# Optimization experiments

Measured on AMD Instinct MI355X. Metric: run time of the kernel, lower is better.

The kernel has to match this reference:

```python
import jax, jax.numpy as jnp
import numpy as np

S, N, C, E, L = 4, 50000, 256, 800000, 3
EPS = 1e-5  # nn.LayerNorm default eps


def setup_inputs() -> dict:
    key = jax.random.key(0)
    ks = jax.random.split(key, 10)
    sc = 1.0 / np.sqrt(C)
    x = jax.random.normal(ks[0], (S, N, C), jnp.float32)
    edge_index = jax.random.randint(ks[1], (S, 2, E), 0, N, dtype=jnp.int32)
    edge_weight = jax.random.uniform(ks[2], (S, E), jnp.float32)
    W_gcn = jax.random.uniform(ks[3], (L, C, C), jnp.float32, -sc, sc)
    b_gcn = jnp.zeros((L, C), jnp.float32)
    ln_scale = jnp.ones((L, C), jnp.float32)
    ln_bias = jnp.zeros((L, C), jnp.float32)
    w_ih = jax.random.uniform(ks[4], (3 * C, C), jnp.float32, -sc, sc)
    w_hh = jax.random.uniform(ks[5], (3 * C, C), jnp.float32, -sc, sc)
    b_ih = jax.random.uniform(ks[6], (3 * C,), jnp.float32, -sc, sc)
    b_hh = jax.random.uniform(ks[7], (3 * C,), jnp.float32, -sc, sc)
    return dict(x=x, edge_index=edge_index, edge_weight=edge_weight,
                W_gcn=W_gcn, b_gcn=b_gcn, ln_scale=ln_scale, ln_bias=ln_bias,
                w_ih=w_ih, w_hh=w_hh, b_ih=b_ih, b_hh=b_hh)


def _gcn_conv(h, row, col, ew, W, b):
    """PyG GCNConv: out = D^{-1/2} (A + I) D^{-1/2} (h W) + b, edge weights ew."""
    h = h @ W  # [N, C]
    loop = jnp.arange(N, dtype=row.dtype)
    row = jnp.concatenate([row, loop])
    col = jnp.concatenate([col, loop])
    ew = jnp.concatenate([ew, jnp.ones((N,), ew.dtype)])
    deg = jax.ops.segment_sum(ew, col, num_segments=N)  # in-degree at targets
    dinv = jnp.where(deg > 0, jax.lax.rsqrt(jnp.maximum(deg, EPS * 0 + 1e-12)), 0.0)
    norm = dinv[row] * ew * dinv[col]  # [E+N]
    msg = h[row] * norm[:, None]       # gather from sources
    return jax.ops.segment_sum(msg, col, num_segments=N) + b


def _layernorm(h, scale, bias):
    mu = jnp.mean(h, axis=-1, keepdims=True)
    var = jnp.mean(jnp.square(h - mu), axis=-1, keepdims=True)
    return (h - mu) * jax.lax.rsqrt(var + EPS) * scale + bias


def _snapshot(x, ei, ew, W_gcn, b_gcn, ln_scale, ln_bias):
    h = x
    row, col = ei[0], ei[1]
    for l in range(L):
        h = _gcn_conv(h, row, col, ew, W_gcn[l], b_gcn[l])
        h = _layernorm(h, ln_scale[l], ln_bias[l])
        h = jax.nn.relu(h)  # dropout is identity in eval mode
    return h


def _gru_last(seq, w_ih, w_hh, b_ih, b_hh):
    """seq: [S, N, C] -> final hidden [N, C] (torch single-layer GRU)."""
    def step(h, x_t):
        gi = x_t @ w_ih.T + b_ih
        gh = h @ w_hh.T + b_hh
        i_r, i_z, i_n = jnp.split(gi, 3, axis=-1)
        h_r, h_z, h_n = jnp.split(gh, 3, axis=-1)
        r = jax.nn.sigmoid(i_r + h_r)
        z = jax.nn.sigmoid(i_z + h_z)
        n = jnp.tanh(i_n + r * h_n)
        return (1.0 - z) * n + z * h, None
    h0 = jnp.zeros(seq.shape[1:], seq.dtype)
    h_last, _ = jax.lax.scan(step, h0, seq)
    return h_last


def reference(x, edge_index, edge_weight, W_gcn, b_gcn, ln_scale, ln_bias,
              w_ih, w_hh, b_ih, b_hh):
    feats = jax.vmap(lambda xs, eis, ews: _snapshot(xs, eis, ews, W_gcn, b_gcn, ln_scale, ln_bias))(
        x, edge_index, edge_weight)  # [S, N, C]
    return _gru_last(feats, w_ih, w_hh, b_ih, b_hh)  # [N, C]
```

## Files before the change

### kernel.cpp

```cpp
#include <hip/hip_runtime.h>
#include <cmath>

#define S_ 4
#define N_ 50000
#define C_ 256
#define E_ 800000
#define L_ 3
#define EPS_ 1e-5f
#define CAP_ 64

typedef __attribute__((ext_vector_type(8))) short bf16x8;
typedef __attribute__((ext_vector_type(4))) float f32x4;

__device__ __forceinline__ float bf2f(unsigned short s) {
  return __uint_as_float(((unsigned)s) << 16);
}
__device__ __forceinline__ unsigned short f2bf(float f) {
  unsigned u = __float_as_uint(f);
  return (unsigned short)((u + 0x7fffu + ((u >> 16) & 1u)) >> 16);
}

__device__ __forceinline__ void gload_lds16(const void* g, void* l) {
  __builtin_amdgcn_global_load_lds(
      (const __attribute__((address_space(1))) unsigned int*)g,
      (__attribute__((address_space(3))) unsigned int*)l, 16, 0, 0);
}

__device__ __forceinline__ void swz_block(int id, int nbx, int nby, int& bmi, int& bni) {
  const int NB8 = nby * 8;
  int fullb = (nbx >> 3) * NB8;
  if (id < fullb) {
    int g = id / NB8, pp = id - g * NB8;
    bmi = g * 8 + (pp & 7);
    bni = pp >> 3;
  } else {
    int rem = nbx & 7;
    int idp = id - fullb;
    bmi = (nbx & ~7) + idp % rem;
    bni = idp / rem;
  }
}

template<bool AF32>
__global__ __launch_bounds__(256) void gemm_bf16_kernel(
    const unsigned short* __restrict__ A, const float* __restrict__ Af,
    const unsigned short* __restrict__ Bt,
    unsigned short* __restrict__ Cout, int M, int Nn, int K, int nby)
{
  __shared__ alignas(16) unsigned short As[2][128 * 32];
  __shared__ alignas(16) unsigned short Bs[2][128 * 32];
  const int tid = threadIdx.x;
  const int lane = tid & 63;
  const int wid = tid >> 6;
  const int wr = wid >> 1, wc = wid & 1;
  int bmi, bni;
  swz_block(blockIdx.x, gridDim.x / nby, nby, bmi, bni);
  const int bm = bmi * 128, bn = bni * 128;
  const int l15 = lane & 15, l4 = lane >> 4;

  f32x4 acc[4][4] = {};

  int offA[4], offB[4];
  #pragma unroll
  for (int mi = 0; mi < 4; ++mi) {
    int ra = wr * 64 + mi * 16 + l15;
    offA[mi] = ra * 32 + ((l4 ^ ((ra >> 1) & 3)) << 3);
    int rb = wc * 64 + mi * 16 + l15;
    offB[mi] = rb * 32 + ((l4 ^ ((rb >> 1) & 3)) << 3);
  }
  const int rs = tid >> 2;
  const int gs = tid & 3;

  float4 fa[2][2];

  auto loadA_f32 = [&](int k0) {
    #pragma unroll
    for (int t2 = 0; t2 < 2; ++t2) {
      int r = rs + t2 * 64;
      int q = gs ^ ((r >> 1) & 3);
      int arow = bm + r; if (arow >= M) arow = M - 1;
      const float* srcp = &Af[(size_t)arow * K + k0 + q * 8];
      fa[t2][0] = *(const float4*)srcp;
      fa[t2][1] = *(const float4*)(srcp + 4);
    }
  };
  auto writeA_f32 = [&](int buf) {
    #pragma unroll
    for (int t2 = 0; t2 < 2; ++t2) {
      int slot = t2 * 256 + tid;
      union { unsigned short us[8]; bf16x8 v; } u;
      const float* f = (const float*)&fa[t2][0];
      #pragma unroll
      for (int j = 0; j < 8; ++j) u.us[j] = f2bf(f[j]);
      *(bf16x8*)&As[buf][slot * 8] = u.v;
    }
  };
  auto stageA_bf = [&](int buf, int k0) {
    #pragma unroll
    for (int t2 = 0; t2 < 2; ++t2) {
      int r = rs + t2 * 64;
      int q = gs ^ ((r >> 1) & 3);
      int arow = bm + r; if (arow >= M) arow = M - 1;
      gload_lds16(&A[(size_t)arow * K + k0 + q * 8], &As[buf][(t2 * 256 + tid) * 8]);
    }
  };
  auto stageB = [&](int buf, int k0) {
    #pragma unroll
    for (int t2 = 0; t2 < 2; ++t2) {
      int r = rs + t2 * 64;
      int q = gs ^ ((r >> 1) & 3);
      gload_lds16(&Bt[(size_t)(bn + r) * K + k0 + q * 8], &Bs[buf][(t2 * 256 + tid) * 8]);
    }
  };

  const int nt = K >> 5;
  if constexpr (AF32) {
    loadA_f32(0);
    stageB(0, 0);
    writeA_f32(0);
  } else {
    stageA_bf(0, 0);
    stageB(0, 0);
  }
  asm volatile("s_waitcnt vmcnt(0)" ::: "memory");
  __syncthreads();

  int cur = 0;
  for (int t = 0; t < nt; ++t) {
    if (t + 1 < nt) {
      if constexpr (AF32) {
        loadA_f32((t + 1) * 32);
        stageB(cur ^ 1, (t + 1) * 32);
      } else {
        stageA_bf(cur ^ 1, (t + 1) * 32);
        stageB(cur ^ 1, (t + 1) * 32);
      }
    }

    bf16x8 af[4], bfr[4];
    #pragma unroll
    for (int mi = 0; mi < 4; ++mi) af[mi] = *(const bf16x8*)&As[cur][offA[mi]];
    #pragma unroll
    for (int ni = 0; ni < 4; ++ni) bfr[ni] = *(const bf16x8*)&Bs[cur][offB[ni]];
    #pragma unroll
    for (int mi = 0; mi < 4; ++mi)
      #pragma unroll
      for (int ni = 0; ni < 4; ++ni)
        acc[mi][ni] = __builtin_amdgcn_mfma_f32_16x16x32_bf16(
            bfr[ni], af[mi], acc[mi][ni], 0, 0, 0);

    if constexpr (AF32) {
      if (t + 1 < nt) writeA_f32(cur ^ 1);
    }
    asm volatile("s_waitcnt vmcnt(0)" ::: "memory");
    __syncthreads();
    cur ^= 1;
  }

  #pragma unroll
  for (int mi = 0; mi < 4; ++mi) {
    int row = bm + wr * 64 + mi * 16 + l15;
    if (row < M) {
      #pragma unroll
      for (int ni = 0; ni < 4; ++ni) {
        int colb = bn + wc * 64 + ni * 16 + l4 * 4;
        ushort4 o;
        o.x = f2bf(acc[mi][ni][0]);
        o.y = f2bf(acc[mi][ni][1]);
        o.z = f2bf(acc[mi][ni][2]);
        o.w = f2bf(acc[mi][ni][3]);
        *(ushort4*)&Cout[(size_t)row * Nn + colb] = o;
      }
    }
  }
}

__global__ __launch_bounds__(256) void gru_fused_kernel(
    const unsigned short* __restrict__ feat,
    const unsigned short* __restrict__ hq_in,
    const unsigned short* __restrict__ Wp_ih,
    const unsigned short* __restrict__ Wp_hh,
    const float* __restrict__ b_ih, const float* __restrict__ b_hh,
    unsigned short* __restrict__ hq_out, float* __restrict__ hout,
    int first, int M)
{
  __shared__ alignas(16) unsigned short As[2][128 * 32];
  __shared__ alignas(16) unsigned short Bs[2][96 * 32];
  const int tid = threadIdx.x;
  const int lane = tid & 63;
  const int wv = tid >> 6;
  const int l15 = lane & 15, l4 = lane >> 4;

  int bmi, bni;
  swz_block(blockIdx.x, gridDim.x / 8, 8, bmi, bni);
  const int bm = bmi * 128;
  const int c0 = bni * 32;
  const int brow0 = bni * 96;

  f32x4 acc_i[2][6] = {};
  f32x4 acc_h[2][6] = {};

  int offA[2], offB[6];
  #pragma unroll
  for (int mi = 0; mi < 2; ++mi) {
    int ra = wv * 32 + mi * 16 + l15;
    offA[mi] = ra * 32 + ((l4 ^ ((ra >> 1) & 3)) << 3);
  }
  #pragma unroll
  for (int ni = 0; ni < 6; ++ni) {
    int rb = ni * 16 + l15;
    offB[ni] = rb * 32 + ((l4 ^ ((rb >> 1) & 3)) << 3);
  }

  const int nt = first ? 8 : 16;

  auto stage = [&](int buf, int t) {
    int k0 = (t & 7) * 32;
    const unsigned short* Ap = (t < 8) ? feat : hq_in;
    const unsigned short* Bp = (t < 8) ? Wp_ih : Wp_hh;
    #pragma unroll
    for (int t2 = 0; t2 < 2; ++t2) {
      int slot = t2 * 256 + tid;
      int r = slot >> 2;
      int q = (slot & 3) ^ ((r >> 1) & 3);
      int arow = bm + r; if (arow >= M) arow = M - 1;
      gload_lds16(&Ap[(size_t)arow * 256 + k0 + q * 8], &As[buf][slot * 8]);
    }
    {
      int slot = tid;
      int r = slot >> 2;
      int q = (slot & 3) ^ ((r >> 1) & 3);
      gload_lds16(&Bp[(size_t)(brow0 + r) * 256 + k0 + q * 8], &Bs[buf][slot * 8]);
    }
    if (tid < 128) {
      int slot = 256 + tid;
      int r = slot >> 2;
      int q = (slot & 3) ^ ((r >> 1) & 3);
      gload_lds16(&Bp[(size_t)(brow0 + r) * 256 + k0 + q * 8], &Bs[buf][slot * 8]);
    }
  };

  stage(0, 0);
  asm volatile("s_waitcnt vmcnt(0)" ::: "memory");
  __syncthreads();

  int cur = 0;
  for (int t = 0; t < nt; ++t) {
    if (t + 1 < nt) stage(cur ^ 1, t + 1);

    bf16x8 af[2], bfr[6];
    #pragma unroll
    for (int mi = 0; mi < 2; ++mi) af[mi] = *(const bf16x8*)&As[cur][offA[mi]];
    #pragma unroll
    for (int ni = 0; ni < 6; ++ni) bfr[ni] = *(const bf16x8*)&Bs[cur][offB[ni]];
    if (t < 8) {
      #pragma unroll
      for (int mi = 0; mi < 2; ++mi)
        #pragma unroll
        for (int ni = 0; ni < 6; ++ni)
          acc_i[mi][ni] = __builtin_amdgcn_mfma_f32_16x16x32_bf16(
              bfr[ni], af[mi], acc_i[mi][ni], 0, 0, 0);
    } else {
      #pragma unroll
      for (int mi = 0; mi < 2; ++mi)
        #pragma unroll
        for (int ni = 0; ni < 6; ++ni)
          acc_h[mi][ni] = __builtin_amdgcn_mfma_f32_16x16x32_bf16(
              bfr[ni], af[mi], acc_h[mi][ni], 0, 0, 0);
    }

    asm volatile("s_waitcnt vmcnt(0)" ::: "memory");
    __syncthreads();
    cur ^= 1;
  }

  #pragma unroll
  for (int mi = 0; mi < 2; ++mi) {
    int row = bm + wv * 32 + mi * 16 + l15;
    if (row < M) {
      #pragma unroll
      for (int cni = 0; cni < 2; ++cni) {
        int dc = cni * 16 + l4 * 4;
        int c = c0 + dc;
        float4 bir = *(const float4*)&b_ih[c];
        float4 biz = *(const float4*)&b_ih[256 + c];
        float4 bin = *(const float4*)&b_ih[512 + c];
        float4 bhr = *(const float4*)&b_hh[c];
        float4 bhz = *(const float4*)&b_hh[256 + c];
        float4 bhn = *(const float4*)&b_hh[512 + c];
        float hpv[4] = {0.f, 0.f, 0.f, 0.f};
        if (!first) {
          ushort4 hp = *(const ushort4*)&hq_in[(size_t)row * 256 + c];
          hpv[0] = bf2f(hp.x); hpv[1] = bf2f(hp.y);
          hpv[2] = bf2f(hp.z); hpv[3] = bf2f(hp.w);
        }
        const float* pbir = (const float*)&bir; const float* pbiz = (const float*)&biz;
        const float* pbin = (const float*)&bin; const float* pbhr = (const float*)&bhr;
        const float* pbhz = (const float*)&bhz; const float* pbhn = (const float*)&bhn;
        float hv[4];
        #pragma unroll
        for (int rr = 0; rr < 4; ++rr) {
          float gir = acc_i[mi][0 + cni][rr] + pbir[rr];
          float giz = acc_i[mi][2 + cni][rr] + pbiz[rr];
          float gin = acc_i[mi][4 + cni][rr] + pbin[rr];
          float ghr = (first ? 0.f : acc_h[mi][0 + cni][rr]) + pbhr[rr];
          float ghz = (first ? 0.f : acc_h[mi][2 + cni][rr]) + pbhz[rr];
          float ghn = (first ? 0.f : acc_h[mi][4 + cni][rr]) + pbhn[rr];
          float rg = 1.f / (1.f + expf(-(gir + ghr)));
          float zg = 1.f / (1.f + expf(-(giz + ghz)));
          float ng = tanhf(gin + rg * ghn);
          hv[rr] = (1.f - zg) * ng + zg * hpv[rr];
        }
        if (hq_out) {
          ushort4 o;
          o.x = f2bf(hv[0]); o.y = f2bf(hv[1]); o.z = f2bf(hv[2]); o.w = f2bf(hv[3]);
          *(ushort4*)&hq_out[(size_t)row * 256 + c] = o;
        }
        if (hout) {
          float4 o = make_float4(hv[0], hv[1], hv[2], hv[3]);
          *(float4*)&hout[(size_t)row * 256 + c] = o;
        }
      }
    }
  }
}

__global__ void prep_weights_kernel(const float* __restrict__ W_gcn,
                                    const float* __restrict__ w_ih,
                                    const float* __restrict__ w_hh,
                                    unsigned short* __restrict__ wt_gcn,
                                    unsigned short* __restrict__ wp_ih,
                                    unsigned short* __restrict__ wp_hh) {
  int i = blockIdx.x * blockDim.x + threadIdx.x;
  const int LCC = L_ * C_ * C_, WSZ = 768 * C_;
  if (i < LCC) {
    int l = i / (C_ * C_);
    int rem = i - l * C_ * C_;
    int nn = rem >> 8, k = rem & 255;
    wt_gcn[i] = f2bf(W_gcn[l * C_ * C_ + k * C_ + nn]);
  } else if (i < LCC + 2 * WSZ) {
    int j = i - LCC;
    int which = j / WSZ;
    int d = j - which * WSZ;
    int jrow = d >> 8, k = d & 255;
    int chunk = jrow / 96, jj = jrow - chunk * 96;
    int g = jj >> 5, dc = jj & 31;
    int srow = g * 256 + chunk * 32 + dc;
    float v = which ? w_hh[srow * 256 + k] : w_ih[srow * 256 + k];
    (which ? wp_hh : wp_ih)[d] = f2bf(v);
  }
}

__global__ void scatter_fill_kernel(const int* __restrict__ edge_idx,
                                    const float* __restrict__ edge_w,
                                    unsigned long long* __restrict__ recs,
                                    int* __restrict__ cnt_g) {
  int e = blockIdx.x * blockDim.x + threadIdx.x;
  if (e < S_ * E_) {
    int s = e / E_;
    int ee = e - s * E_;
    int r = edge_idx[(size_t)s * 2 * E_ + ee];
    int c = edge_idx[(size_t)s * 2 * E_ + E_ + ee];
    float w = edge_w[(size_t)s * E_ + ee];
    int ng = s * N_ + c;
    int pos = atomicAdd(&cnt_g[ng], 1);
    if (pos < CAP_) {
      recs[((size_t)ng << 6) + pos] =
          ((unsigned long long)__float_as_uint(w) << 32) | (unsigned int)r;
    }
  }
}

__global__ __launch_bounds__(256) void deg_dinv_kernel(
    const unsigned long long* __restrict__ recs, const int* __restrict__ cnt_g,
    float* __restrict__ dinv_g) {
  const int lane = threadIdx.x & 63, wv = threadIdx.x >> 6;
  const int ng = blockIdx.x * 4 + wv;
  int cnt = min(cnt_g[ng], CAP_);
  float w = 0.f;
  if (lane < cnt)
    w = __uint_as_float((unsigned int)(recs[((size_t)ng << 6) + lane] >> 32));
  #pragma unroll
  for (int off = 32; off > 0; off >>= 1) w += __shfl_xor(w, off);
  if (lane == 0) dinv_g[ng] = rsqrtf(w + 1.0f);
}

__global__ void normify_kernel(const unsigned long long* __restrict__ recs,
                               const int* __restrict__ cnt_g,
                               const float* __restrict__ dinv_g,
                               unsigned int* __restrict__ src_norm) {
  int idx = blockIdx.x * blockDim.x + threadIdx.x;
  if (idx < S_ * N_ * CAP_) {
    int ng = idx >> 6, slot = idx & 63;
    int cnt = min(cnt_g[ng], CAP_);
    if (slot < cnt) {
      unsigned long long rec = recs[idx];
      int src = (int)(unsigned int)rec & 0xFFFF;
      float w = __uint_as_float((unsigned int)(rec >> 32));
      int s = ng / N_;
      float nrm = dinv_g[s * N_ + src] * w * dinv_g[ng];
      src_norm[idx] = (unsigned int)src | ((unsigned int)f2bf(nrm) << 16);
    }
  }
}

__global__ __launch_bounds__(256) void spmm_ln_relu_kernel(
    const unsigned short* __restrict__ hW_all, const int* __restrict__ cnt_g,
    const unsigned int* __restrict__ src_norm, const float* __restrict__ dinv_g,
    const float* __restrict__ bgcn, const float* __restrict__ lnsc,
    const float* __restrict__ lnbi, unsigned short* __restrict__ out)
{
  const int tid = threadIdx.x;
  const int lane = tid & 63, wv = tid >> 6;
  const int n_g = blockIdx.x * 4 + wv;
  const int s = n_g / N_;
  const int n = n_g - s * N_;
  const int c4 = lane << 2;
  const unsigned short* hW = hW_all + ((size_t)s * N_ << 8);

  const int cnt = min(cnt_g[n_g], CAP_);
  unsigned int rec = (lane < cnt) ? src_norm[((size_t)n_g << 6) + lane] : 0u;

  float a0, a1, a2, a3;
  {
    float dv = dinv_g[n_g];
    float w = dv * dv;
    ushort4 u = *(const ushort4*)&hW[((size_t)n << 8) + c4];
    a0 = w * bf2f(u.x); a1 = w * bf2f(u.y); a2 = w * bf2f(u.z); a3 = w * bf2f(u.w);
  }
  int j = 0;
  for (; j + 3 < cnt; j += 4) {
    unsigned int r0 = __shfl((int)rec, j + 0);
    unsigned int r1 = __shfl((int)rec, j + 1);
    unsigned int r2 = __shfl((int)rec, j + 2);
    unsigned int r3 = __shfl((int)rec, j + 3);
    ushort4 u0 = *(const ushort4*)&hW[((size_t)(r0 & 0xFFFFu) << 8) + c4];
    ushort4 u1 = *(const ushort4*)&hW[((size_t)(r1 & 0xFFFFu) << 8) + c4];
    ushort4 u2 = *(const ushort4*)&hW[((size_t)(r2 & 0xFFFFu) << 8) + c4];
    ushort4 u3 = *(const ushort4*)&hW[((size_t)(r3 & 0xFFFFu) << 8) + c4];
    float n0 = bf2f((unsigned short)(r0 >> 16));
    float n1 = bf2f((unsigned short)(r1 >> 16));
    float n2 = bf2f((unsigned short)(r2 >> 16));
    float n3 = bf2f((unsigned short)(r3 >> 16));
    a0 = fmaf(n0, bf2f(u0.x), a0); a1 = fmaf(n0, bf2f(u0.y), a1);
    a2 = fmaf(n0, bf2f(u0.z), a2); a3 = fmaf(n0, bf2f(u0.w), a3);
    a0 = fmaf(n1, bf2f(u1.x), a0); a1 = fmaf(n1, bf2f(u1.y), a1);
    a2 = fmaf(n1, bf2f(u1.z), a2); a3 = fmaf(n1, bf2f(u1.w), a3);
    a0 = fmaf(n2, bf2f(u2.x), a0); a1 = fmaf(n2, bf2f(u2.y), a1);
    a2 = fmaf(n2, bf2f(u2.z), a2); a3 = fmaf(n2, bf2f(u2.w), a3);
    a0 = fmaf(n3, bf2f(u3.x), a0); a1 = fmaf(n3, bf2f(u3.y), a1);
    a2 = fmaf(n3, bf2f(u3.z), a2); a3 = fmaf(n3, bf2f(u3.w), a3);
  }
  for (; j < cnt; ++j) {
    unsigned int r0 = __shfl((int)rec, j);
    ushort4 u0 = *(const ushort4*)&hW[((size_t)(r0 & 0xFFFFu) << 8) + c4];
    float n0 = bf2f((unsigned short)(r0 >> 16));
    a0 = fmaf(n0, bf2f(u0.x), a0); a1 = fmaf(n0, bf2f(u0.y), a1);
    a2 = fmaf(n0, bf2f(u0.z), a2); a3 = fmaf(n0, bf2f(u0.w), a3);
  }

  float4 bg = *(const float4*)&bgcn[c4];
  float v0 = a0 + bg.x, v1 = a1 + bg.y, v2 = a2 + bg.z, v3 = a3 + bg.w;
  float s1 = (v0 + v1) + (v2 + v3);
  float s2 = (v0 * v0 + v1 * v1) + (v2 * v2 + v3 * v3);
  #pragma unroll
  for (int off = 32; off > 0; off >>= 1) {
    s1 += __shfl_xor(s1, off);
    s2 += __shfl_xor(s2, off);
  }
  float mu = s1 * (1.0f / C_);
  float var = s2 * (1.0f / C_) - mu * mu;
  float inv = rsqrtf(var + EPS_);
  float4 sc = *(const float4*)&lnsc[c4];
  float4 bi = *(const float4*)&lnbi[c4];
  ushort4 o;
  o.x = f2bf(fmaxf((v0 - mu) * inv * sc.x + bi.x, 0.f));
  o.y = f2bf(fmaxf((v1 - mu) * inv * sc.y + bi.y, 0.f));
  o.z = f2bf(fmaxf((v2 - mu) * inv * sc.z + bi.z, 0.f));
  o.w = f2bf(fmaxf((v3 - mu) * inv * sc.w + bi.w, 0.f));
  *(ushort4*)&out[((size_t)n_g << 8) + c4] = o;
}

extern "C" void kernel_launch(void* const* d_in, const int* in_sizes, int n_in,
                              void* d_out, int out_size, void* d_ws, size_t ws_size,
                              hipStream_t stream) {
  const float* x        = (const float*)d_in[0];
  const int*   edge_idx = (const int*)d_in[1];
  const float* edge_w   = (const float*)d_in[2];
  const float* W_gcn    = (const float*)d_in[3];
  const float* b_gcn    = (const float*)d_in[4];
  const float* ln_scale = (const float*)d_in[5];
  const float* ln_bias  = (const float*)d_in[6];
  const float* w_ih     = (const float*)d_in[7];
  const float* w_hh     = (const float*)d_in[8];
  const float* b_ih     = (const float*)d_in[9];
  const float* b_hh     = (const float*)d_in[10];
  float* h_out = (float*)d_out;

  char* p = (char*)d_ws;
  auto carve = [&](size_t bytes) -> void* {
    void* r = (void*)p;
    p += (bytes + 255) & ~(size_t)255;
    return r;
  };
  unsigned long long* recs = (unsigned long long*)carve((size_t)S_ * N_ * CAP_ * 8);
  unsigned int* src_norm = (unsigned int*)carve((size_t)S_ * N_ * CAP_ * 4);
  int*   cnt_g       = (int*)carve((size_t)S_ * N_ * 4);
  float* dinv_g      = (float*)carve((size_t)S_ * N_ * 4);
  unsigned short* wt_gcn = (unsigned short*)carve((size_t)L_ * C_ * C_ * 2);
  unsigned short* wp_ih  = (unsigned short*)carve((size_t)768 * C_ * 2);
  unsigned short* wp_hh  = (unsigned short*)carve((size_t)768 * C_ * 2);
  unsigned short* hW_all = (unsigned short*)carve((size_t)S_ * N_ * C_ * 2);
  unsigned short* fA_all = (unsigned short*)carve((size_t)S_ * N_ * C_ * 2);
  unsigned short* fB_all = (unsigned short*)carve((size_t)S_ * N_ * C_ * 2);
  unsigned short* hq0    = (unsigned short*)carve((size_t)N_ * C_ * 2);
  unsigned short* hq1    = (unsigned short*)carve((size_t)N_ * C_ * 2);

  const int TB = 256;

  hipMemsetAsync(cnt_g, 0, (size_t)S_ * N_ * 4, stream);

  const int PREP_N = L_ * C_ * C_ + 2 * 768 * C_;
  prep_weights_kernel<<<(PREP_N + TB - 1) / TB, TB, 0, stream>>>(
      W_gcn, w_ih, w_hh, wt_gcn, wp_ih, wp_hh);

  scatter_fill_kernel<<<(S_ * E_ + TB - 1) / TB, TB, 0, stream>>>(
      edge_idx, edge_w, recs, cnt_g);
  deg_dinv_kernel<<<S_ * N_ / 4, TB, 0, stream>>>(recs, cnt_g, dinv_g);
  normify_kernel<<<(S_ * N_ * CAP_ + TB - 1) / TB, TB, 0, stream>>>(
      recs, cnt_g, dinv_g, src_norm);

  const int M_all = S_ * N_;
  const int nbx = (M_all + 127) / 128;
  {
    unsigned short* louts[3] = {fA_all, fB_all, fA_all};
    const unsigned short* hin = nullptr;
    for (int l = 0; l < L_; ++l) {
      if (l == 0) {
        gemm_bf16_kernel<true><<<nbx * (C_ / 128), 256, 0, stream>>>(
            nullptr, x, wt_gcn, hW_all, M_all, C_, C_, C_ / 128);
      } else {
        gemm_bf16_kernel<false><<<nbx * (C_ / 128), 256, 0, stream>>>(
            hin, nullptr, wt_gcn + (size_t)l * C_ * C_, hW_all, M_all, C_, C_, C_ / 128);
      }
      spmm_ln_relu_kernel<<<M_all / 4, 256, 0, stream>>>(
          hW_all, cnt_g, src_norm, dinv_g, b_gcn + l * C_,
          ln_scale + l * C_, ln_bias + l * C_, louts[l]);
      hin = louts[l];
    }
  }
  const unsigned short* feat_all = fA_all;

  const int gnb = ((N_ + 127) / 128) * 8;
  unsigned short* hq_cur = hq0;
  unsigned short* hq_nxt = hq1;
  for (int s = 0; s < S_; ++s) {
    bool last = (s == S_ - 1);
    gru_fused_kernel<<<gnb, 256, 0, stream>>>(
        feat_all + (size_t)s * N_ * C_,
        hq_cur,
        wp_ih, wp_hh, b_ih, b_hh,
        last ? nullptr : hq_nxt,
        last ? h_out : nullptr,
        (s == 0) ? 1 : 0, N_);
    unsigned short* t = hq_cur; hq_cur = hq_nxt; hq_nxt = t;
  }
}
```

Measured before the change: 1.563 ms.

## Shard edge scatter by destination range and pack records into 32-bit words

The scatter kernel becomes a grid-stride loop where each block handles one of eight destination-node shards, so atomics and record writes for a shard hit a smaller region of memory and get better cache locality. Edge records are packed into 32 bits (16-bit source plus bf16 weight) instead of 64 bits, and normify now rewrites them in place, which removes the separate src_norm buffer. The trade-off is that every block reads the full column array eight times. Storing the raw edge weight as bf16 also loses some precision in the degree sums.

New measurement: 1.482 ms, median of 2. 1.05x faster.

```diff
diff --git a/kernel.cpp b/kernel.cpp
--- a/kernel.cpp
+++ b/kernel.cpp
@@ -8,6 +8,8 @@
 #define L_ 3
 #define EPS_ 1e-5f
 #define CAP_ 64
+#define NSHARD_ 8
+#define SHARD_N_ (N_ / NSHARD_)
 
 typedef __attribute__((ext_vector_type(8))) short bf16x8;
 typedef __attribute__((ext_vector_type(4))) float f32x4;
@@ -280,8 +282,7 @@
     if (row < M) {
       #pragma unroll
       for (int cni = 0; cni < 2; ++cni) {
-        int dc = cni * 16 + l4 * 4;
-        int c = c0 + dc;
+        int c = c0 + cni * 16 + l4 * 4;
         float4 bir = *(const float4*)&b_ih[c];
         float4 biz = *(const float4*)&b_ih[256 + c];
         float4 bin = *(const float4*)&b_ih[512 + c];
@@ -351,55 +352,60 @@
   }
 }
 
-__global__ void scatter_fill_kernel(const int* __restrict__ edge_idx,
-                                    const float* __restrict__ edge_w,
-                                    unsigned long long* __restrict__ recs,
-                                    int* __restrict__ cnt_g) {
-  int e = blockIdx.x * blockDim.x + threadIdx.x;
-  if (e < S_ * E_) {
-    int s = e / E_;
-    int ee = e - s * E_;
-    int r = edge_idx[(size_t)s * 2 * E_ + ee];
-    int c = edge_idx[(size_t)s * 2 * E_ + E_ + ee];
-    float w = edge_w[(size_t)s * E_ + ee];
-    int ng = s * N_ + c;
-    int pos = atomicAdd(&cnt_g[ng], 1);
-    if (pos < CAP_) {
-      recs[((size_t)ng << 6) + pos] =
-          ((unsigned long long)__float_as_uint(w) << 32) | (unsigned int)r;
+__global__ __launch_bounds__(256) void scatter_fill_kernel(
+    const int* __restrict__ edge_idx, const float* __restrict__ edge_w,
+    unsigned int* __restrict__ recs, int* __restrict__ cnt_g) {
+  const int tid = threadIdx.x;
+  const int shard = blockIdx.x & (NSHARD_ - 1);
+  const int bidx = blockIdx.x >> 3;
+  const int nblk = gridDim.x >> 3;
+  const int lo = shard * SHARD_N_, hi = lo + SHARD_N_;
+  for (int s = 0; s < S_; ++s) {
+    const int* row = edge_idx + (size_t)s * 2 * E_;
+    const int* col = row + E_;
+    const float* ew = edge_w + (size_t)s * E_;
+    for (int e = bidx * 256 + tid; e < E_; e += nblk * 256) {
+      int c = col[e];
+      if (c >= lo && c < hi) {
+        int ng = s * N_ + c;
+        int pos = atomicAdd(&cnt_g[ng], 1);
+        if (pos < CAP_) {
+          recs[((size_t)ng << 6) + pos] =
+              (unsigned int)row[e] | ((unsigned int)f2bf(ew[e]) << 16);
+        }
+      }
     }
   }
 }
 
 __global__ __launch_bounds__(256) void deg_dinv_kernel(
-    const unsigned long long* __restrict__ recs, const int* __restrict__ cnt_g,
+    const unsigned int* __restrict__ recs, const int* __restrict__ cnt_g,
     float* __restrict__ dinv_g) {
   const int lane = threadIdx.x & 63, wv = threadIdx.x >> 6;
   const int ng = blockIdx.x * 4 + wv;
   int cnt = min(cnt_g[ng], CAP_);
   float w = 0.f;
   if (lane < cnt)
-    w = __uint_as_float((unsigned int)(recs[((size_t)ng << 6) + lane] >> 32));
+    w = bf2f((unsigned short)(recs[((size_t)ng << 6) + lane] >> 16));
   #pragma unroll
   for (int off = 32; off > 0; off >>= 1) w += __shfl_xor(w, off);
   if (lane == 0) dinv_g[ng] = rsqrtf(w + 1.0f);
 }
 
-__global__ void normify_kernel(const unsigned long long* __restrict__ recs,
+__global__ void normify_kernel(unsigned int* __restrict__ recs,
                                const int* __restrict__ cnt_g,
-                               const float* __restrict__ dinv_g,
-                               unsigned int* __restrict__ src_norm) {
+                               const float* __restrict__ dinv_g) {
   int idx = blockIdx.x * blockDim.x + threadIdx.x;
   if (idx < S_ * N_ * CAP_) {
     int ng = idx >> 6, slot = idx & 63;
     int cnt = min(cnt_g[ng], CAP_);
     if (slot < cnt) {
-      unsigned long long rec = recs[idx];
-      int src = (int)(unsigned int)rec & 0xFFFF;
-      float w = __uint_as_float((unsigned int)(rec >> 32));
+      unsigned int rec = recs[idx];
+      int src = (int)(rec & 0xFFFFu);
+      float w = bf2f((unsigned short)(rec >> 16));
       int s = ng / N_;
       float nrm = dinv_g[s * N_ + src] * w * dinv_g[ng];
-      src_norm[idx] = (unsigned int)src | ((unsigned int)f2bf(nrm) << 16);
+      recs[idx] = (rec & 0xFFFFu) | ((unsigned int)f2bf(nrm) << 16);
     }
   }
 }
@@ -503,8 +509,7 @@
     p += (bytes + 255) & ~(size_t)255;
     return r;
   };
-  unsigned long long* recs = (unsigned long long*)carve((size_t)S_ * N_ * CAP_ * 8);
-  unsigned int* src_norm = (unsigned int*)carve((size_t)S_ * N_ * CAP_ * 4);
+  unsigned int* recs = (unsigned int*)carve((size_t)S_ * N_ * CAP_ * 4);
   int*   cnt_g       = (int*)carve((size_t)S_ * N_ * 4);
   float* dinv_g      = (float*)carve((size_t)S_ * N_ * 4);
   unsigned short* wt_gcn = (unsigned short*)carve((size_t)L_ * C_ * C_ * 2);
@@ -524,11 +529,10 @@
   prep_weights_kernel<<<(PREP_N + TB - 1) / TB, TB, 0, stream>>>(
       W_gcn, w_ih, w_hh, wt_gcn, wp_ih, wp_hh);
 
-  scatter_fill_kernel<<<(S_ * E_ + TB - 1) / TB, TB, 0, stream>>>(
-      edge_idx, edge_w, recs, cnt_g);
+  scatter_fill_kernel<<<2048, TB, 0, stream>>>(edge_idx, edge_w, recs, cnt_g);
   deg_dinv_kernel<<<S_ * N_ / 4, TB, 0, stream>>>(recs, cnt_g, dinv_g);
   normify_kernel<<<(S_ * N_ * CAP_ + TB - 1) / TB, TB, 0, stream>>>(
-      recs, cnt_g, dinv_g, src_norm);
+      recs, cnt_g, dinv_g);
 
   const int M_all = S_ * N_;
   const int nbx = (M_all + 127) / 128;
@@ -544,7 +548,7 @@
             hin, nullptr, wt_gcn + (size_t)l * C_ * C_, hW_all, M_all, C_, C_, C_ / 128);
       }
       spmm_ln_relu_kernel<<<M_all / 4, 256, 0, stream>>>(
-          hW_all, cnt_g, src_norm, dinv_g, b_gcn + l * C_,
+          hW_all, cnt_g, recs, dinv_g, b_gcn + l * C_,
           ln_scale + l * C_, ln_bias + l * C_, louts[l]);
       hin = louts[l];
     }
```
